# Kernel optimization log

Measured on AMD Instinct MI355X. Metric: run time of the kernel, lower is better.

## Reference

```python
import jax, jax.numpy as jnp
import numpy as np

B, V, N, C, H = 4, 8, 256, 768, 12
DH = C // H
NEG = -1e9


def setup_inputs() -> dict:
    key = jax.random.key(0)
    k0, k1, k2, k3, k4, k5 = jax.random.split(key, 6)
    feats = jax.random.normal(k0, (B, V, N, C), dtype=jnp.float32)
    is_ref = jax.random.randint(k1, (B, V), 0, 2).astype(bool)
    # nn.MultiheadAttention params: packed in_proj (3C, C) + bias, out_proj Linear(C, C)
    w_qkv = jax.random.normal(k2, (3 * C, C), dtype=jnp.float32) * 0.02
    b_qkv = jax.random.normal(k3, (3 * C,), dtype=jnp.float32) * 0.02
    w_out = jax.random.normal(k4, (C, C), dtype=jnp.float32) * 0.02
    b_out = jax.random.normal(k5, (C,), dtype=jnp.float32) * 0.02
    return {"feats": feats, "is_ref": is_ref, "w_qkv": w_qkv, "b_qkv": b_qkv,
            "w_out": w_out, "b_out": b_out}


def reference(feats, is_ref, w_qkv, b_qkv, w_out, b_out):
    b_, v_, n_, c_ = feats.shape
    # packed QKV projection (torch Linear: x @ W.T + b)
    qkv = feats @ w_qkv.T + b_qkv                      # (B,V,N,3C)
    q, k, v = jnp.split(qkv, 3, axis=-1)
    q = q.reshape(b_, v_, n_, H, DH) * (1.0 / jnp.sqrt(jnp.float32(DH)))
    k = k.reshape(b_, v_ * n_, H, DH)                  # keys flattened over views
    v = v.reshape(b_, v_ * n_, H, DH)
    # view v attends to views w with opposite ref flag
    allowed = is_ref[:, :, None] ^ is_ref[:, None, :]  # (B,V,V) bool
    key_mask = jnp.repeat(allowed, n_, axis=2)         # (B,V,V*N)
    scores = jnp.einsum('bvnhd,bmhd->bhvnm', q, k)     # (B,H,V,N,V*N)
    logits = jnp.where(key_mask[:, None, :, None, :], scores, NEG)
    attn = jax.nn.softmax(logits, axis=-1)
    ctx = jnp.einsum('bhvnm,bmhd->bvnhd', attn, v).reshape(b_, v_, n_, c_)
    out = ctx @ w_out.T + b_out
    # views with empty context pass through unchanged
    has_ctx = allowed.any(axis=-1)                     # (B,V)
    return jnp.where(has_ctx[:, :, None, None], out, feats)
```

## Files before the change

### kernel.cpp

```cpp
#include <hip/hip_runtime.h>
#include <hip/hip_bf16.h>
#include <math.h>

#define BDIM 4
#define VDIM 8
#define NDIM 256
#define CDIM 768
#define HDIM 12
#define DHE  64
#define C3   (3*CDIM)
#define ROWS (BDIM*VDIM*NDIM)
#define KEYS (VDIM*NDIM)

typedef __attribute__((ext_vector_type(8))) short short8;
typedef __attribute__((ext_vector_type(4))) float float4v;

__device__ inline unsigned short f2bf(float f) {
    unsigned int u = __builtin_bit_cast(unsigned int, f);
    u += 0x7fffu + ((u >> 16) & 1u);
    return (unsigned short)(u >> 16);
}

__device__ __forceinline__ unsigned int pk2(float a, float b) {
    return (unsigned int)f2bf(a) | ((unsigned int)f2bf(b) << 16);
}

__device__ __forceinline__ uint4 pk8(float4 a, float4 b) {
    uint4 r;
    r.x = pk2(a.x, a.y); r.y = pk2(a.z, a.w);
    r.z = pk2(b.x, b.y); r.w = pk2(b.z, b.w);
    return r;
}

__device__ __forceinline__ void gld_lds16(const unsigned short* g, unsigned short* l) {
    __builtin_amdgcn_global_load_lds(
        (const __attribute__((address_space(1))) void*)g,
        (__attribute__((address_space(3))) void*)l, 16, 0, 0);
}

#define NA8 786432
#define NW8 221184
#define NO8 73728

__global__ __launch_bounds__(256) void cast_bf16_all(
    const float* __restrict__ fA, const float* __restrict__ fW,
    const float* __restrict__ fO,
    unsigned short* __restrict__ bA, unsigned short* __restrict__ bW,
    unsigned short* __restrict__ bO)
{
    const int gid = blockIdx.x * 256 + threadIdx.x;
    const float* src;
    unsigned short* dst;
    int idx;
    if (gid < NA8)            { src = fA; dst = bA; idx = gid; }
    else if (gid < NA8 + NW8) { src = fW; dst = bW; idx = gid - NA8; }
    else                      { src = fO; dst = bO; idx = gid - NA8 - NW8; }
    const float4* p = (const float4*)(src + (size_t)idx * 8);
    *(uint4*)(dst + (size_t)idx * 8) = pk8(p[0], p[1]);
}

__global__ __launch_bounds__(256) void gemm_qkv_mfma(
    const unsigned short* __restrict__ A,
    const unsigned short* __restrict__ W,
    const float* __restrict__ bias,
    unsigned short* __restrict__ out,
    unsigned short* __restrict__ vT)
{
    __shared__ __attribute__((aligned(16))) unsigned short As[128][32];
    __shared__ __attribute__((aligned(16))) unsigned short Ws[128][32];
    const int t = threadIdx.x;
    const int wave = t >> 6, lane = t & 63;
    const int m = lane & 15, quad = lane >> 4;
    const int wr = (wave >> 1) * 64, wc = (wave & 1) * 64;
    const int row0 = blockIdx.y * 128, col0 = blockIdx.x * 128;

    const int sr = t >> 2, sk = (t & 3) * 8;
    const unsigned short* ag = &A[(size_t)(row0 + sr) * CDIM + sk];
    const unsigned short* wg = &W[(size_t)(col0 + sr) * CDIM + sk];
    unsigned short* la0 = &As[sr][sk];
    unsigned short* la1 = &As[64 + sr][sk];
    unsigned short* lw0 = &Ws[sr][sk];
    unsigned short* lw1 = &Ws[64 + sr][sk];

    float4v acc[4][4] = {};

    for (int k0 = 0; k0 < CDIM; k0 += 32) {
        gld_lds16(ag + k0, la0);
        gld_lds16(ag + (size_t)64 * CDIM + k0, la1);
        gld_lds16(wg + k0, lw0);
        gld_lds16(wg + (size_t)64 * CDIM + k0, lw1);
        __syncthreads();
        short8 a[4], b[4];
        #pragma unroll
        for (int rt = 0; rt < 4; rt++)
            a[rt] = *(const short8*)&As[wr + rt * 16 + m][quad * 8];
        #pragma unroll
        for (int ct = 0; ct < 4; ct++)
            b[ct] = *(const short8*)&Ws[wc + ct * 16 + m][quad * 8];
        #pragma unroll
        for (int rt = 0; rt < 4; rt++)
            #pragma unroll
            for (int ct = 0; ct < 4; ct++)
                acc[rt][ct] = __builtin_amdgcn_mfma_f32_16x16x32_bf16(
                    a[rt], b[ct], acc[rt][ct], 0, 0, 0);
        __syncthreads();
    }

    if (col0 < 2 * CDIM) {
        #pragma unroll
        for (int ct = 0; ct < 4; ct++) {
            const int col = col0 + wc + ct * 16 + m;
            const float bv = bias[col];
            #pragma unroll
            for (int rt = 0; rt < 4; rt++) {
                const size_t row = (size_t)row0 + wr + rt * 16 + quad * 4;
                #pragma unroll
                for (int r = 0; r < 4; r++)
                    out[(row + r) * C3 + col] = f2bf(acc[rt][ct][r] + bv);
            }
        }
    } else {
        #pragma unroll
        for (int ct = 0; ct < 4; ct++) {
            const int vcol = col0 + wc + ct * 16 + m - 2 * CDIM;
            const int h = vcol >> 6, d = vcol & 63;
            const float bv = bias[col0 + wc + ct * 16 + m];
            #pragma unroll
            for (int rt = 0; rt < 4; rt++) {
                const int row = row0 + wr + rt * 16 + quad * 4;
                const int bidx = row >> 11, key = row & 2047;
                ushort4 pkv;
                pkv.x = f2bf(acc[rt][ct][0] + bv);
                pkv.y = f2bf(acc[rt][ct][1] + bv);
                pkv.z = f2bf(acc[rt][ct][2] + bv);
                pkv.w = f2bf(acc[rt][ct][3] + bv);
                *(ushort4*)&vT[((size_t)(bidx * HDIM + h) * DHE + d) * KEYS + key] = pkv;
            }
        }
    }
}

__global__ __launch_bounds__(256, 3) void attn_mfma(
    const unsigned short* __restrict__ qkv,
    const unsigned short* __restrict__ vT,
    const int* __restrict__ is_ref,
    unsigned short* __restrict__ ctx)
{
    const int g = blockIdx.x;
    const int round = g >> 8, cu = g & 255;
    const int idx = (round & 1) ? ((round << 8) | (255 - cu)) : g;

    int rmask[4], r4[4];
    #pragma unroll
    for (int bb = 0; bb < 4; bb++) {
        int mask = 0;
        #pragma unroll
        for (int w = 0; w < VDIM; w++)
            if (is_ref[bb * VDIM + w] != 0) mask |= 1 << w;
        rmask[bb] = mask; r4[bb] = __popc(mask);
    }
    int rr = idx, b = 0, nv = 0, Lsel = 0;
    bool found = false;
    for (int Lc = 8; Lc >= 0 && !found; Lc--) {
        for (int bb = 0; bb < 4 && !found; bb++) {
            int n = 0;
            if (8 - r4[bb] == Lc) n += r4[bb];
            if (r4[bb] == Lc) n += 8 - r4[bb];
            if (rr < 24 * n) { b = bb; nv = n; Lsel = Lc; found = true; }
            else rr -= 24 * n;
        }
    }
    const int h = rr / (2 * nv);
    const int rem = rr % (2 * nv);
    const int half = rem / nv;
    int pos = rem % nv;
    int S = 0;
    if (8 - r4[b] == Lsel) S |= rmask[b];
    if (r4[b] == Lsel) S |= (~rmask[b]) & 0xff;
    int v = 0;
    for (int vv = 0; vv < 8; vv++) {
        if ((S >> vv) & 1) { if (pos == 0) { v = vv; break; } pos--; }
    }

    const int t = threadIdx.x, wave = t >> 6, lane = t & 63;
    const int m = lane & 15, quad = lane >> 4;
    const int n0 = half * 128 + wave * 32;

    __shared__ unsigned short Ks[128][64];
    __shared__ unsigned short Vs[64][128];
    __shared__ unsigned short Ps[4][32][72];

    const int my_ref = (rmask[b] >> v) & 1;
    const unsigned amask = my_ref ? (unsigned)((~rmask[b]) & 0xff)
                                  : (unsigned)rmask[b];
    const int nChunks = 2 * Lsel;

    const float c1 = 0.18033688f;

    short8 aq[2][2];
    #pragma unroll
    for (int qt = 0; qt < 2; qt++) {
        const size_t row = (size_t)((b * VDIM + v) * NDIM) + n0 + qt * 16 + m;
        #pragma unroll
        for (int ks = 0; ks < 2; ks++)
            aq[qt][ks] = *(const short8*)&qkv[row * C3 + h * DHE + ks * 32 + quad * 8];
    }

    float rs[2] = {0.f, 0.f};
    float4v O[2][4] = {};

    const int k_key = t >> 3, k_dg = t & 7;
    const int v_dim = t >> 4, v_kg = t & 15;

    const unsigned short* vTb = vT + (size_t)(b * HDIM + h) * DHE * KEYS;

    uint4 kreg[4], vreg[4];
    unsigned rem2 = amask;
    int wcur = __builtin_ffs((int)rem2) - 1;

    if (nChunks > 0) {
        const unsigned short* kb =
            qkv + (size_t)((b * VDIM + wcur) * NDIM) * C3 + CDIM + h * DHE;
        #pragma unroll
        for (int i = 0; i < 4; i++)
            kreg[i] = *(const uint4*)&kb[(size_t)(i * 32 + k_key) * C3 + k_dg * 8];
        #pragma unroll
        for (int i = 0; i < 4; i++)
            vreg[i] = *(const uint4*)&vTb[(size_t)(i * 16 + v_dim) * KEYS
                                          + wcur * NDIM + v_kg * 8];
    }

    for (int ci = 0; ci < nChunks; ci++) {
        __syncthreads();
        #pragma unroll
        for (int i = 0; i < 4; i++)
            *(uint4*)&Ks[i * 32 + k_key][(k_dg ^ (k_key & 7)) * 8] = kreg[i];
        #pragma unroll
        for (int i = 0; i < 4; i++)
            *(uint4*)&Vs[i * 16 + v_dim][(v_kg ^ v_dim) * 8] = vreg[i];

        if (ci + 1 < nChunks) {
            int wn, m0n;
            if ((ci & 1) == 0) { wn = wcur; m0n = 128; }
            else {
                unsigned r2 = rem2 & (rem2 - 1);
                wn = __builtin_ffs((int)r2) - 1; m0n = 0;
            }
            const unsigned short* kb =
                qkv + (size_t)((b * VDIM + wn) * NDIM + m0n) * C3 + CDIM + h * DHE;
            #pragma unroll
            for (int i = 0; i < 4; i++)
                kreg[i] = *(const uint4*)&kb[(size_t)(i * 32 + k_key) * C3 + k_dg * 8];
            #pragma unroll
            for (int i = 0; i < 4; i++)
                vreg[i] = *(const uint4*)&vTb[(size_t)(i * 16 + v_dim) * KEYS
                                              + wn * NDIM + m0n + v_kg * 8];
        }
        __syncthreads();

        #pragma unroll
        for (int hk = 0; hk < 2; hk++) {
            #pragma unroll
            for (int kt = 0; kt < 4; kt++) {
                const int nt = hk * 4 + kt;
                const short8 bk0 = *(const short8*)&Ks[nt * 16 + m][(quad ^ (m & 7)) * 8];
                const short8 bk1 = *(const short8*)&Ks[nt * 16 + m][((4 + quad) ^ (m & 7)) * 8];
                #pragma unroll
                for (int qt = 0; qt < 2; qt++) {
                    float4v s = {};
                    s = __builtin_amdgcn_mfma_f32_16x16x32_bf16(bk0, aq[qt][0], s, 0, 0, 0);
                    s = __builtin_amdgcn_mfma_f32_16x16x32_bf16(bk1, aq[qt][1], s, 0, 0, 0);
                    const float p0 = __builtin_amdgcn_exp2f(s[0] * c1);
                    const float p1 = __builtin_amdgcn_exp2f(s[1] * c1);
                    const float p2 = __builtin_amdgcn_exp2f(s[2] * c1);
                    const float p3 = __builtin_amdgcn_exp2f(s[3] * c1);
                    rs[qt] += (p0 + p1) + (p2 + p3);
                    uint2 pw;
                    pw.x = pk2(p0, p1);
                    pw.y = pk2(p2, p3);
                    *(uint2*)&Ps[wave][qt * 16 + m][kt * 16 + quad * 4] = pw;
                }
            }
            #pragma unroll
            for (int kk = 0; kk < 2; kk++) {
                const short8 ap0 = *(const short8*)&Ps[wave][m][kk * 32 + quad * 8];
                const short8 ap1 = *(const short8*)&Ps[wave][16 + m][kk * 32 + quad * 8];
                #pragma unroll
                for (int ct = 0; ct < 4; ct++) {
                    const short8 bv = *(const short8*)&Vs[ct * 16 + m]
                        [((hk * 8 + kk * 4 + quad) ^ m) * 8];
                    O[0][ct] = __builtin_amdgcn_mfma_f32_16x16x32_bf16(ap0, bv, O[0][ct], 0, 0, 0);
                    O[1][ct] = __builtin_amdgcn_mfma_f32_16x16x32_bf16(ap1, bv, O[1][ct], 0, 0, 0);
                }
            }
        }
        if (ci & 1) { rem2 &= rem2 - 1; wcur = __builtin_ffs((int)rem2) - 1; }
    }

    #pragma unroll
    for (int qt = 0; qt < 2; qt++) {
        float x = rs[qt];
        x += __shfl_xor(x, 16, 64);
        x += __shfl_xor(x, 32, 64);
        const float inv = (x > 0.f) ? 1.f / x : 0.f;
        float invq[4];
        #pragma unroll
        for (int r = 0; r < 4; r++)
            invq[r] = __shfl(inv, quad * 4 + r, 64);
        const size_t rowg = (size_t)((b * VDIM + v) * NDIM) + n0 + qt * 16 + quad * 4;
        #pragma unroll
        for (int ct = 0; ct < 4; ct++)
            #pragma unroll
            for (int r = 0; r < 4; r++)
                ctx[(rowg + r) * CDIM + h * DHE + ct * 16 + m] = f2bf(O[qt][ct][r] * invq[r]);
    }
}

__global__ __launch_bounds__(256) void gemm_out_mfma(
    const unsigned short* __restrict__ A,
    const unsigned short* __restrict__ W,
    const float* __restrict__ bias,
    const float* __restrict__ feats,
    const int* __restrict__ is_ref,
    float* __restrict__ out)
{
    __shared__ __attribute__((aligned(16))) unsigned short As[128][32];
    __shared__ __attribute__((aligned(16))) unsigned short Ws[128][32];
    const int t = threadIdx.x;
    const int wave = t >> 6, lane = t & 63;
    const int m = lane & 15, quad = lane >> 4;
    const int wr = (wave >> 1) * 64, wc = (wave & 1) * 64;
    const int row0 = blockIdx.y * 128, col0 = blockIdx.x * 128;

    const int sr = t >> 2, sk = (t & 3) * 8;
    const unsigned short* ag = &A[(size_t)(row0 + sr) * CDIM + sk];
    const unsigned short* wg = &W[(size_t)(col0 + sr) * CDIM + sk];
    unsigned short* la0 = &As[sr][sk];
    unsigned short* la1 = &As[64 + sr][sk];
    unsigned short* lw0 = &Ws[sr][sk];
    unsigned short* lw1 = &Ws[64 + sr][sk];

    float4v acc[4][4] = {};

    for (int k0 = 0; k0 < CDIM; k0 += 32) {
        gld_lds16(ag + k0, la0);
        gld_lds16(ag + (size_t)64 * CDIM + k0, la1);
        gld_lds16(wg + k0, lw0);
        gld_lds16(wg + (size_t)64 * CDIM + k0, lw1);
        __syncthreads();
        short8 a[4], b[4];
        #pragma unroll
        for (int rt = 0; rt < 4; rt++)
            a[rt] = *(const short8*)&As[wr + rt * 16 + m][quad * 8];
        #pragma unroll
        for (int ct = 0; ct < 4; ct++)
            b[ct] = *(const short8*)&Ws[wc + ct * 16 + m][quad * 8];
        #pragma unroll
        for (int rt = 0; rt < 4; rt++)
            #pragma unroll
            for (int ct = 0; ct < 4; ct++)
                acc[rt][ct] = __builtin_amdgcn_mfma_f32_16x16x32_bf16(
                    a[rt], b[ct], acc[rt][ct], 0, 0, 0);
        __syncthreads();
    }

    const int bidx = row0 / (VDIM * NDIM);
    const int vidx = (row0 / NDIM) % VDIM;
    const int my = is_ref[bidx * VDIM + vidx];
    bool has = false;
    #pragma unroll
    for (int w = 0; w < VDIM; w++) has = has || (is_ref[bidx * VDIM + w] != my);

    #pragma unroll
    for (int ct = 0; ct < 4; ct++) {
        const int col = col0 + wc + ct * 16 + m;
        const float bv = bias[col];
        #pragma unroll
        for (int rt = 0; rt < 4; rt++) {
            const size_t row = (size_t)row0 + wr + rt * 16 + quad * 4;
            #pragma unroll
            for (int r = 0; r < 4; r++) {
                float o = acc[rt][ct][r] + bv;
                if (!has) o = feats[(row + r) * CDIM + col];
                out[(row + r) * CDIM + col] = o;
            }
        }
    }
}

extern "C" void kernel_launch(void* const* d_in, const int* in_sizes, int n_in,
                              void* d_out, int out_size, void* d_ws, size_t ws_size,
                              hipStream_t stream) {
    const float* feats = (const float*)d_in[0];
    const int*   is_ref = (const int*)d_in[1];
    const float* w_qkv = (const float*)d_in[2];
    const float* b_qkv = (const float*)d_in[3];
    const float* w_out = (const float*)d_in[4];
    const float* b_out = (const float*)d_in[5];
    float* out = (float*)d_out;

    unsigned short* qkv_b = (unsigned short*)d_ws;
    unsigned short* vT    = qkv_b + (size_t)ROWS * C3;
    unsigned short* ctx_b = vT + (size_t)BDIM * HDIM * DHE * KEYS;
    unsigned short* A_bf  = ctx_b + (size_t)ROWS * CDIM;
    unsigned short* Wq_bf = A_bf + (size_t)ROWS * CDIM;
    unsigned short* Wo_bf = Wq_bf + (size_t)C3 * CDIM;

    cast_bf16_all<<<dim3((NA8 + NW8 + NO8) / 256), 256, 0, stream>>>(
        feats, w_qkv, w_out, A_bf, Wq_bf, Wo_bf);

    dim3 g1(C3 / 128, ROWS / 128);
    gemm_qkv_mfma<<<g1, 256, 0, stream>>>(A_bf, Wq_bf, b_qkv, qkv_b, vT);

    attn_mfma<<<dim3(768), 256, 0, stream>>>(qkv_b, vT, is_ref, ctx_b);

    dim3 g3(CDIM / 128, ROWS / 128);
    gemm_out_mfma<<<g3, 256, 0, stream>>>(ctx_b, Wo_bf, b_out, feats, is_ref, out);
    (void)in_sizes; (void)n_in; (void)out_size; (void)ws_size;
}
```

Before: 251.8 us.

## Remap attention blocks so each XCD handles fixed (batch, head) groups

Changes the block-to-work mapping in the attention kernel. Blocks are grouped by the low 3 bits of the block id, which on MI355X round-robins across 8 XCDs. Each group gets a balanced subset of (batch, head) pairs, with batches sorted by workload and assigned in snake order, so K/V for a head stays in one XCD's L2. Within each group blocks are still ordered longest-first with an alternating sweep. This adds index computation per block and assumes the grid covers exactly 48 groups times the per-group block count.

Result: faster. 245.9 us (-2.4%).

```diff
diff --git a/kernel.cpp b/kernel.cpp
--- a/kernel.cpp
+++ b/kernel.cpp
@@ -147,8 +147,8 @@
     unsigned short* __restrict__ ctx)
 {
     const int g = blockIdx.x;
-    const int round = g >> 8, cu = g & 255;
-    const int idx = (round & 1) ? ((round << 8) | (255 - cu)) : g;
+    const int myx = g & 7, cuu = (g >> 3) & 31, round = g >> 8;
+    const int j = round * 32 + ((round & 1) ? (31 - cuu) : cuu);
 
     int rmask[4], r4[4];
     #pragma unroll
@@ -159,27 +159,42 @@
             if (is_ref[bb * VDIM + w] != 0) mask |= 1 << w;
         rmask[bb] = mask; r4[bb] = __popc(mask);
     }
-    int rr = idx, b = 0, nv = 0, Lsel = 0;
-    bool found = false;
-    for (int Lc = 8; Lc >= 0 && !found; Lc--) {
-        for (int bb = 0; bb < 4 && !found; bb++) {
-            int n = 0;
-            if (8 - r4[bb] == Lc) n += r4[bb];
-            if (r4[bb] == Lc) n += 8 - r4[bb];
-            if (rr < 24 * n) { b = bb; nv = n; Lsel = Lc; found = true; }
-            else rr -= 24 * n;
-        }
-    }
-    const int h = rr / (2 * nv);
-    const int rem = rr % (2 * nv);
-    const int half = rem / nv;
-    int pos = rem % nv;
-    int S = 0;
-    if (8 - r4[b] == Lsel) S |= rmask[b];
-    if (r4[b] == Lsel) S |= (~rmask[b]) & 0xff;
-    int v = 0;
-    for (int vv = 0; vv < 8; vv++) {
-        if ((S >> vv) & 1) { if (pos == 0) { v = vv; break; } pos--; }
+    int ord[4] = {0, 1, 2, 3};
+    #pragma unroll
+    for (int i = 0; i < 3; i++)
+        #pragma unroll
+        for (int k = 0; k < 3 - i; k++) {
+            const int wa = r4[ord[k]] * (8 - r4[ord[k]]);
+            const int wb = r4[ord[k + 1]] * (8 - r4[ord[k + 1]]);
+            if (wb > wa) { int tmp = ord[k]; ord[k] = ord[k + 1]; ord[k + 1] = tmp; }
+        }
+    int Gb[6], Gh[6], ng = 0;
+    for (int p = 0; p < 48; p++) {
+        const int row = p >> 3, col = p & 7;
+        const int x = (row & 1) ? (7 - col) : col;
+        if (x == myx) { Gb[ng] = ord[p / 12]; Gh[ng] = p % 12; ng++; }
+    }
+    int b = 0, h = 0, half = 0, v = 0, Lsel = 0;
+    {
+        int jj = j;
+        bool found = false;
+        for (int o = 8; o >= 0 && !found; o--) {
+            for (int gi = 0; gi < 6 && !found; gi++) {
+                const int b2 = Gb[gi], r2 = r4[b2];
+                const int nv_o = ((8 - r2) == o ? r2 : 0) + (r2 == o ? (8 - r2) : 0);
+                const int cnt = 2 * nv_o;
+                if (cnt > 0 && jj < cnt) {
+                    b = b2; h = Gh[gi]; Lsel = o;
+                    half = jj / nv_o;
+                    int pos = jj % nv_o;
+                    int S = (((8 - r2) == o) ? rmask[b2] : 0)
+                          | ((r2 == o) ? ((~rmask[b2]) & 0xff) : 0);
+                    for (int vv = 0; vv < 8; vv++)
+                        if ((S >> vv) & 1) { if (pos == 0) { v = vv; break; } pos--; }
+                    found = true;
+                } else jj -= cnt;
+            }
+        }
     }
 
     const int t = threadIdx.x, wave = t >> 6, lane = t & 63;
```
